# Performance work log

Hardware: AMD Instinct MI355X
Metric: run time of the kernel (lower is better)

The kernel has to match this reference:

```python
import jax, jax.numpy as jnp
import numpy as np

N, C, F, T = 8, 4, 257, 2000
B = 8            # spatial_filters (beams)
M = 80           # spectra_filters
EPS = 1e-5


def setup_inputs() -> dict:
    key = jax.random.key(0)
    ks = jax.random.split(key, 10)
    scale = 0.1
    return {
        "x_real": jax.random.normal(ks[0], (N, C, F, T), jnp.float32),
        "x_imag": jax.random.normal(ks[1], (N, C, F, T), jnp.float32),
        # query beamformer (1 beam): conv weights per bin, shape (F, 1, C)
        "wq_r": jax.random.normal(ks[2], (F, 1, C), jnp.float32) * scale,
        "wq_i": jax.random.normal(ks[3], (F, 1, C), jnp.float32) * scale,
        # key/value beamformers: (F, B, C)
        "wk_r": jax.random.normal(ks[4], (F, B, C), jnp.float32) * scale,
        "wk_i": jax.random.normal(ks[5], (F, B, C), jnp.float32) * scale,
        "wv_r": jax.random.normal(ks[6], (F, B, C), jnp.float32) * scale,
        "wv_i": jax.random.normal(ks[7], (F, B, C), jnp.float32) * scale,
        # spectra projection Linear(F -> M, bias=False): torch weight (M, F)
        "proj_w": jax.random.normal(ks[8], (M, F), jnp.float32) * (1.0 / np.sqrt(F)),
        # BatchNorm1d(M) affine params
        "bn_gamma": jnp.ones((M,), jnp.float32),
        "bn_beta": jnp.zeros((M,), jnp.float32),
    }


def _complex_beam_abs(xr, xi, wr, wi):
    # xr/xi: (N,T,F,C); wr/wi: (F,Beams,C)
    # grouped per-bin conv with kernel==length reduces to contraction over C
    rr = jnp.einsum("ntfc,fbc->ntfb", xr, wr)
    ii = jnp.einsum("ntfc,fbc->ntfb", xi, wi)
    ri = jnp.einsum("ntfc,fbc->ntfb", xi, wr)
    ir = jnp.einsum("ntfc,fbc->ntfb", xr, wi)
    br = rr - ii
    bi = ri + ir
    return jnp.sqrt(br * br + bi * bi + EPS)


def reference(x_real, x_imag, wq_r, wq_i, wk_r, wk_i, wv_r, wv_i, proj_w, bn_gamma, bn_beta):
    # N,C,F,T -> N,T,F,C
    xr = jnp.transpose(x_real, (0, 3, 2, 1))
    xi = jnp.transpose(x_imag, (0, 3, 2, 1))
    bq = _complex_beam_abs(xr, xi, wq_r, wq_i)[..., 0]   # (N,T,F)
    bk = _complex_beam_abs(xr, xi, wk_r, wk_i)           # (N,T,F,B)
    bv = _complex_beam_abs(xr, xi, wv_r, wv_i)           # (N,T,F,B)
    s = jnp.sum(bq[..., None] * bk, axis=-2)             # (N,T,B)
    s = jnp.mean(s, axis=-2, keepdims=True)              # (N,1,B) time-invariant
    w = jax.nn.softmax(s, axis=-1)                       # (N,1,B)
    v = jnp.sum(w[:, None] * bv, axis=-1)                # (N,T,F)
    f = jax.nn.relu(jnp.einsum("ntf,mf->ntm", v, proj_w))
    f = jnp.log(f + EPS)                                 # (N,T,M)
    # BatchNorm1d over channel dim M, training-mode batch stats (biased var)
    mu = jnp.mean(f, axis=(0, 1))
    var = jnp.var(f, axis=(0, 1))
    f = (f - mu) * jax.lax.rsqrt(var + EPS) * bn_gamma + bn_beta
    return f
```

## Files before the change

### kernel.cpp

```cpp
#include <hip/hip_runtime.h>
#include <math.h>

#define NN 8
#define CC 4
#define FF 257
#define TT 2000
#define BB 8
#define MM 80
#define EPSF 1e-5f
#define T4N 500
#define PTILE 32
#define PSTR 260
#define PCHUNK 63

typedef float v2f __attribute__((ext_vector_type(2)));

__device__ __forceinline__ float fsqrt_fast(float x) { return __builtin_amdgcn_sqrtf(x); }
__device__ __forceinline__ float flog_fast(float x)  { return __builtin_amdgcn_logf(x) * 0.69314718055994531f; }
__device__ __forceinline__ v2f sqrt2(v2f m) {
    v2f r; r.x = __builtin_amdgcn_sqrtf(m.x); r.y = __builtin_amdgcn_sqrtf(m.y); return r;
}

__global__ __launch_bounds__(256) void k_beam_s(
    const float* __restrict__ xr_g, const float* __restrict__ xi_g,
    const float* __restrict__ wq_r, const float* __restrict__ wq_i,
    const float* __restrict__ wk_r, const float* __restrict__ wk_i,
    float* __restrict__ s_buf)
{
    int nf = blockIdx.x;
    int n = nf / FF, f = nf % FF;
    int t4 = blockIdx.y * 256 + threadIdx.x;

    float part[BB];
#pragma unroll
    for (int b = 0; b < BB; ++b) part[b] = 0.f;

    if (t4 < T4N) {
        const float* xr_base = xr_g + ((size_t)(n*CC)*FF + f) * TT + t4*4;
        const float* xi_base = xi_g + ((size_t)(n*CC)*FF + f) * TT + t4*4;
        v2f xr2[CC][2], xi2[CC][2];
#pragma unroll
        for (int c = 0; c < CC; ++c) {
            float4 r4 = *reinterpret_cast<const float4*>(xr_base + (size_t)c*FF*TT);
            float4 i4 = *reinterpret_cast<const float4*>(xi_base + (size_t)c*FF*TT);
            xr2[c][0].x = r4.x; xr2[c][0].y = r4.y; xr2[c][1].x = r4.z; xr2[c][1].y = r4.w;
            xi2[c][0].x = i4.x; xi2[c][0].y = i4.y; xi2[c][1].x = i4.z; xi2[c][1].y = i4.w;
        }

        const float4 qr4 = *reinterpret_cast<const float4*>(&wq_r[f*CC]);
        const float4 qi4 = *reinterpret_cast<const float4*>(&wq_i[f*CC]);

        v2f qq[2];
#pragma unroll
        for (int p = 0; p < 2; ++p) {
            v2f qr = xr2[0][p]*qr4.x + xr2[1][p]*qr4.y + xr2[2][p]*qr4.z + xr2[3][p]*qr4.w
                   - xi2[0][p]*qi4.x - xi2[1][p]*qi4.y - xi2[2][p]*qi4.z - xi2[3][p]*qi4.w;
            v2f qi = xi2[0][p]*qr4.x + xi2[1][p]*qr4.y + xi2[2][p]*qr4.z + xi2[3][p]*qr4.w
                   + xr2[0][p]*qi4.x + xr2[1][p]*qi4.y + xr2[2][p]*qi4.z + xr2[3][p]*qi4.w;
            qq[p] = qr*qr + qi*qi + EPSF;
        }

#pragma unroll
        for (int b = 0; b < BB; ++b) {
            const float4 wr4 = *reinterpret_cast<const float4*>(&wk_r[(f*BB + b)*CC]);
            const float4 wi4 = *reinterpret_cast<const float4*>(&wk_i[(f*BB + b)*CC]);
            v2f acc; acc.x = 0.f; acc.y = 0.f;
#pragma unroll
            for (int p = 0; p < 2; ++p) {
                v2f kr = xr2[0][p]*wr4.x + xr2[1][p]*wr4.y + xr2[2][p]*wr4.z + xr2[3][p]*wr4.w
                       - xi2[0][p]*wi4.x - xi2[1][p]*wi4.y - xi2[2][p]*wi4.z - xi2[3][p]*wi4.w;
                v2f ki = xi2[0][p]*wr4.x + xi2[1][p]*wr4.y + xi2[2][p]*wr4.z + xi2[3][p]*wr4.w
                       + xr2[0][p]*wi4.x + xr2[1][p]*wi4.y + xr2[2][p]*wi4.z + xr2[3][p]*wi4.w;
                v2f kk = kr*kr + ki*ki + EPSF;
                acc += sqrt2(qq[p] * kk);
            }
            part[b] = acc.x + acc.y;
        }
    }

    __shared__ float red[4][BB];
    int lane = threadIdx.x & 63, wv = threadIdx.x >> 6;
#pragma unroll
    for (int b = 0; b < BB; ++b) {
        float v = part[b];
#pragma unroll
        for (int m = 32; m >= 1; m >>= 1) v += __shfl_xor(v, m);
        if (lane == 0) red[wv][b] = v;
    }
    __syncthreads();
    if (threadIdx.x < BB) {
        float v = red[0][threadIdx.x] + red[1][threadIdx.x]
                + red[2][threadIdx.x] + red[3][threadIdx.x];
        int bin = (blockIdx.x * 2 + blockIdx.y) & 15;
        atomicAdd(&s_buf[bin*64 + n*BB + threadIdx.x], v);
    }
}

__global__ void k_softmax(const float* __restrict__ s_buf, float* __restrict__ w_buf)
{
    int tid = threadIdx.x;
    if (tid < NN*BB) {
        float v = 0.f;
#pragma unroll
        for (int j = 0; j < 16; ++j) v += s_buf[j*64 + tid];
        v *= (1.0f / TT);
        float mx = v;
#pragma unroll
        for (int m = 4; m >= 1; m >>= 1) mx = fmaxf(mx, __shfl_xor(mx, m));
        float e = expf(v - mx);
        float sm = e;
#pragma unroll
        for (int m = 4; m >= 1; m >>= 1) sm += __shfl_xor(sm, m);
        w_buf[tid] = e / sm;
    }
}

__global__ void k_prep(const float* __restrict__ proj_w, float* __restrict__ proj_pad)
{
    int i = blockIdx.x * 256 + threadIdx.x;
    if (i < MM * 260) {
        int m = i / 260, f = i % 260;
        proj_pad[i] = (f < FF) ? proj_w[m*FF + f] : 0.f;
    }
}

__global__ __launch_bounds__(256) void k_vcompute(
    const float* __restrict__ xr_g, const float* __restrict__ xi_g,
    const float* __restrict__ wv_r, const float* __restrict__ wv_i,
    const float* __restrict__ w_buf, float* __restrict__ vbuf)
{
    int nf = blockIdx.x;
    int n = nf / FF, f = nf % FF;
    int t4 = blockIdx.y * 256 + threadIdx.x;
    if (t4 >= T4N) return;

    const float* xr_base = xr_g + ((size_t)(n*CC)*FF + f) * TT + t4*4;
    const float* xi_base = xi_g + ((size_t)(n*CC)*FF + f) * TT + t4*4;
    v2f xr2[CC][2], xi2[CC][2];
#pragma unroll
    for (int c = 0; c < CC; ++c) {
        float4 r4 = *reinterpret_cast<const float4*>(xr_base + (size_t)c*FF*TT);
        float4 i4 = *reinterpret_cast<const float4*>(xi_base + (size_t)c*FF*TT);
        xr2[c][0].x = r4.x; xr2[c][0].y = r4.y; xr2[c][1].x = r4.z; xr2[c][1].y = r4.w;
        xi2[c][0].x = i4.x; xi2[c][0].y = i4.y; xi2[c][1].x = i4.z; xi2[c][1].y = i4.w;
    }

    v2f vo[2];
    vo[0].x = 0.f; vo[0].y = 0.f; vo[1].x = 0.f; vo[1].y = 0.f;
#pragma unroll
    for (int b = 0; b < BB; ++b) {
        float wn = w_buf[n*BB + b];
        const float4 wr4 = *reinterpret_cast<const float4*>(&wv_r[(f*BB + b)*CC]);
        const float4 wi4 = *reinterpret_cast<const float4*>(&wv_i[(f*BB + b)*CC]);
#pragma unroll
        for (int p = 0; p < 2; ++p) {
            v2f vr = xr2[0][p]*wr4.x + xr2[1][p]*wr4.y + xr2[2][p]*wr4.z + xr2[3][p]*wr4.w
                   - xi2[0][p]*wi4.x - xi2[1][p]*wi4.y - xi2[2][p]*wi4.z - xi2[3][p]*wi4.w;
            v2f vi = xi2[0][p]*wr4.x + xi2[1][p]*wr4.y + xi2[2][p]*wr4.z + xi2[3][p]*wr4.w
                   + xr2[0][p]*wi4.x + xr2[1][p]*wi4.y + xr2[2][p]*wi4.z + xr2[3][p]*wi4.w;
            vo[p] += wn * sqrt2(vr*vr + vi*vi + EPSF);
        }
    }
    float4 o; o.x = vo[0].x; o.y = vo[0].y; o.z = vo[1].x; o.w = vo[1].y;
    *reinterpret_cast<float4*>(&vbuf[((size_t)(n*FF + f))*TT + t4*4]) = o;
}

__global__ __launch_bounds__(256) void k_proj(
    const float* __restrict__ vbuf, const float* __restrict__ proj_pad,
    float* __restrict__ out, double* __restrict__ bn_sum, double* __restrict__ bn_sumsq)
{
    __shared__ float v_lds[PTILE * PSTR];
    int n = blockIdx.x, chunk = blockIdx.y;
    int t0 = chunk * PTILE;
    int tid = threadIdx.x;
    bool full = (t0 + PTILE <= TT);

    if (tid < PTILE*3) {
        int t = tid / 3, fp = FF + tid % 3;
        v_lds[t*PSTR + fp] = 0.f;
    }

    int tq = tid & 7, fi = tid >> 3;
    bool tqv = full || (tq < 4);
#pragma unroll
    for (int k = 0; k < 8; ++k) {
        int f = fi + 32*k;
        float4 vv;
        if (tqv) vv = *reinterpret_cast<const float4*>(&vbuf[((size_t)(n*FF + f))*TT + t0 + tq*4]);
        else { vv.x = 0.f; vv.y = 0.f; vv.z = 0.f; vv.w = 0.f; }
        v_lds[(tq*4 + 0)*PSTR + f] = vv.x;
        v_lds[(tq*4 + 1)*PSTR + f] = vv.y;
        v_lds[(tq*4 + 2)*PSTR + f] = vv.z;
        v_lds[(tq*4 + 3)*PSTR + f] = vv.w;
    }
    if (tid < 8) {
        float4 vv;
        if (full || tid < 4) vv = *reinterpret_cast<const float4*>(&vbuf[((size_t)(n*FF + 256))*TT + t0 + tid*4]);
        else { vv.x = 0.f; vv.y = 0.f; vv.z = 0.f; vv.w = 0.f; }
        v_lds[(tid*4 + 0)*PSTR + 256] = vv.x;
        v_lds[(tid*4 + 1)*PSTR + 256] = vv.y;
        v_lds[(tid*4 + 2)*PSTR + 256] = vv.z;
        v_lds[(tid*4 + 3)*PSTR + 256] = vv.w;
    }
    __syncthreads();

    int tl = tid & 7, fg = tid >> 3;
    int mstart = (fg >> 1)*5 + ((fg & 1) ? 3 : 0);
    bool three = !(fg & 1);

    v2f acc[3][4];
#pragma unroll
    for (int mi = 0; mi < 3; ++mi)
#pragma unroll
        for (int j = 0; j < 4; ++j) { acc[mi][j].x = 0.f; acc[mi][j].y = 0.f; }

    const float* pp = proj_pad + mstart*260;
#pragma unroll 2
    for (int f4 = 0; f4 < 260; f4 += 4) {
        float4 p0 = *reinterpret_cast<const float4*>(&pp[f4]);
        float4 p1 = *reinterpret_cast<const float4*>(&pp[260 + f4]);
        v2f q00, q01, q10, q11, q20, q21;
        q00.x = p0.x; q00.y = p0.y; q01.x = p0.z; q01.y = p0.w;
        q10.x = p1.x; q10.y = p1.y; q11.x = p1.z; q11.y = p1.w;
        if (three) {
            float4 p2 = *reinterpret_cast<const float4*>(&pp[520 + f4]);
            q20.x = p2.x; q20.y = p2.y; q21.x = p2.z; q21.y = p2.w;
        }
#pragma unroll
        for (int j = 0; j < 4; ++j) {
            float4 vv = *reinterpret_cast<const float4*>(&v_lds[(tl + 8*j)*PSTR + f4]);
            v2f v0, v1;
            v0.x = vv.x; v0.y = vv.y; v1.x = vv.z; v1.y = vv.w;
            acc[0][j] += v0*q00 + v1*q01;
            acc[1][j] += v0*q10 + v1*q11;
            if (three) acc[2][j] += v0*q20 + v1*q21;
        }
    }

    int bin = chunk & 15;
#pragma unroll
    for (int mi = 0; mi < 3; ++mi) {
        if (mi == 2 && !three) break;
        int m = mstart + mi;
        float s1 = 0.f, s2 = 0.f;
#pragma unroll
        for (int j = 0; j < 4; ++j) {
            int t = t0 + tl + 8*j;
            if (t < TT) {
                float r = flog_fast(fmaxf(acc[mi][j].x + acc[mi][j].y, 0.f) + EPSF);
                s1 += r; s2 += r*r;
                out[((size_t)n*TT + t)*MM + m] = r;
            }
        }
#pragma unroll
        for (int msk = 4; msk >= 1; msk >>= 1) {
            s1 += __shfl_xor(s1, msk);
            s2 += __shfl_xor(s2, msk);
        }
        if (tl == 0) {
            atomicAdd(&bn_sum[bin*MM + m], (double)s1);
            atomicAdd(&bn_sumsq[bin*MM + m], (double)s2);
        }
    }
}

__global__ void k_bnprep(const double* __restrict__ bn_sum, const double* __restrict__ bn_sumsq,
                         const float* __restrict__ gamma, const float* __restrict__ beta,
                         float* __restrict__ scale, float* __restrict__ shift)
{
    int m = threadIdx.x;
    if (m < MM) {
        double s = 0.0, q = 0.0;
#pragma unroll
        for (int j = 0; j < 16; ++j) { s += bn_sum[j*MM + m]; q += bn_sumsq[j*MM + m]; }
        double inv = 1.0 / (double)(NN * TT);
        double mu = s * inv;
        double var = q * inv - mu * mu;
        float sc = gamma[m] * rsqrtf((float)var + EPSF);
        scale[m] = sc;
        shift[m] = beta[m] - (float)mu * sc;
    }
}

__global__ __launch_bounds__(256) void k_bnapply(float* __restrict__ out,
                                                 const float* __restrict__ scale,
                                                 const float* __restrict__ shift)
{
    int i4 = blockIdx.x * 256 + threadIdx.x;
    if (i4 < NN*TT*MM/4) {
        float4 v = *reinterpret_cast<const float4*>(&out[i4*4]);
        int m = (i4*4) % MM;
        v.x = v.x*scale[m+0] + shift[m+0];
        v.y = v.y*scale[m+1] + shift[m+1];
        v.z = v.z*scale[m+2] + shift[m+2];
        v.w = v.w*scale[m+3] + shift[m+3];
        *reinterpret_cast<float4*>(&out[i4*4]) = v;
    }
}

extern "C" void kernel_launch(void* const* d_in, const int* in_sizes, int n_in,
                              void* d_out, int out_size, void* d_ws, size_t ws_size,
                              hipStream_t stream)
{
    const float* x_real   = (const float*)d_in[0];
    const float* x_imag   = (const float*)d_in[1];
    const float* wq_r     = (const float*)d_in[2];
    const float* wq_i     = (const float*)d_in[3];
    const float* wk_r     = (const float*)d_in[4];
    const float* wk_i     = (const float*)d_in[5];
    const float* wv_r     = (const float*)d_in[6];
    const float* wv_i     = (const float*)d_in[7];
    const float* proj_w   = (const float*)d_in[8];
    const float* bn_gamma = (const float*)d_in[9];
    const float* bn_beta  = (const float*)d_in[10];
    float* out = (float*)d_out;

    char* ws = (char*)d_ws;
    float*  s_buf    = (float*)(ws + 0);
    float*  w_buf    = (float*)(ws + 4096);
    float*  scale    = (float*)(ws + 4352);
    float*  shift    = (float*)(ws + 4672);
    double* bn_sum   = (double*)(ws + 8192);
    double* bn_sumsq = (double*)(ws + 18432);
    float*  proj_pad = (float*)(ws + 28672);
    float*  vbuf     = (float*)(ws + 112640);

    hipMemsetAsync(d_ws, 0, 28672, stream);

    k_prep<<<(MM*260 + 255)/256, 256, 0, stream>>>(proj_w, proj_pad);

    dim3 g1(NN*FF, 2);
    k_beam_s<<<g1, 256, 0, stream>>>(x_real, x_imag, wq_r, wq_i, wk_r, wk_i, s_buf);

    k_softmax<<<1, 64, 0, stream>>>(s_buf, w_buf);

    k_vcompute<<<g1, 256, 0, stream>>>(x_real, x_imag, wv_r, wv_i, w_buf, vbuf);

    dim3 g3(NN, PCHUNK);
    k_proj<<<g3, 256, 0, stream>>>(vbuf, proj_pad, out, bn_sum, bn_sumsq);

    k_bnprep<<<1, 128, 0, stream>>>(bn_sum, bn_sumsq, bn_gamma, bn_beta, scale, shift);

    k_bnapply<<<(NN*TT*MM/4 + 255)/256, 256, 0, stream>>>(out, scale, shift);
}
```

Measured before the change: 101.2 us.

## Fuse small kernels and apply batch-norm via cooperative grid sync

Cuts seven launches down to three. The proj_w padding moves into the beam-score kernel, and each vcompute block computes the softmax itself. The projection kernel becomes a cooperative launch that syncs the whole grid and then applies the batch-norm scale and shift to its own tile while it is likely still in cache. The beam kernels now process both time halves per thread with a 1D grid, which doubles the work per thread and leaves 6 of 256 threads idle. The goal is to remove launch gaps and one full pass over the output, at the cost of grid-sync overhead, per-block recomputation of the softmax, and fewer blocks in flight for the beam kernels.

```diff
diff --git a/kernel.cpp b/kernel.cpp
--- a/kernel.cpp
+++ b/kernel.cpp
@@ -1,5 +1,8 @@
 #include <hip/hip_runtime.h>
+#include <hip/hip_cooperative_groups.h>
 #include <math.h>
+
+namespace cg = cooperative_groups;
 
 #define NN 8
 #define CC 4
@@ -8,10 +11,10 @@
 #define BB 8
 #define MM 80
 #define EPSF 1e-5f
-#define T4N 500
 #define PTILE 32
 #define PSTR 260
 #define PCHUNK 63
+#define HALF1 1000
 
 typedef float v2f __attribute__((ext_vector_type(2)));
 
@@ -25,39 +28,53 @@
     const float* __restrict__ xr_g, const float* __restrict__ xi_g,
     const float* __restrict__ wq_r, const float* __restrict__ wq_i,
     const float* __restrict__ wk_r, const float* __restrict__ wk_i,
-    float* __restrict__ s_buf)
+    float* __restrict__ s_buf,
+    const float* __restrict__ proj_w, float* __restrict__ proj_pad)
 {
     int nf = blockIdx.x;
+    int tid = threadIdx.x;
+
+    {
+        int i = nf*256 + tid;
+        if (i < MM*260) {
+            int m = i/260, fp = i%260;
+            proj_pad[i] = (fp < FF) ? proj_w[m*FF + fp] : 0.f;
+        }
+    }
+
     int n = nf / FF, f = nf % FF;
-    int t4 = blockIdx.y * 256 + threadIdx.x;
 
     float part[BB];
 #pragma unroll
     for (int b = 0; b < BB; ++b) part[b] = 0.f;
 
-    if (t4 < T4N) {
-        const float* xr_base = xr_g + ((size_t)(n*CC)*FF + f) * TT + t4*4;
-        const float* xi_base = xi_g + ((size_t)(n*CC)*FF + f) * TT + t4*4;
-        v2f xr2[CC][2], xi2[CC][2];
+    if (tid < 250) {
+        size_t base0 = ((size_t)(n*CC)*FF + f)*TT + tid*4;
+        v2f xr2[CC][2][2], xi2[CC][2][2];
 #pragma unroll
         for (int c = 0; c < CC; ++c) {
-            float4 r4 = *reinterpret_cast<const float4*>(xr_base + (size_t)c*FF*TT);
-            float4 i4 = *reinterpret_cast<const float4*>(xi_base + (size_t)c*FF*TT);
-            xr2[c][0].x = r4.x; xr2[c][0].y = r4.y; xr2[c][1].x = r4.z; xr2[c][1].y = r4.w;
-            xi2[c][0].x = i4.x; xi2[c][0].y = i4.y; xi2[c][1].x = i4.z; xi2[c][1].y = i4.w;
+#pragma unroll
+            for (int h = 0; h < 2; ++h) {
+                float4 r4 = *reinterpret_cast<const float4*>(xr_g + base0 + (size_t)c*FF*TT + h*HALF1);
+                float4 i4 = *reinterpret_cast<const float4*>(xi_g + base0 + (size_t)c*FF*TT + h*HALF1);
+                xr2[c][h][0].x = r4.x; xr2[c][h][0].y = r4.y; xr2[c][h][1].x = r4.z; xr2[c][h][1].y = r4.w;
+                xi2[c][h][0].x = i4.x; xi2[c][h][0].y = i4.y; xi2[c][h][1].x = i4.z; xi2[c][h][1].y = i4.w;
+            }
         }
 
         const float4 qr4 = *reinterpret_cast<const float4*>(&wq_r[f*CC]);
         const float4 qi4 = *reinterpret_cast<const float4*>(&wq_i[f*CC]);
 
-        v2f qq[2];
+        v2f qq[2][2];
+#pragma unroll
+        for (int h = 0; h < 2; ++h)
 #pragma unroll
         for (int p = 0; p < 2; ++p) {
-            v2f qr = xr2[0][p]*qr4.x + xr2[1][p]*qr4.y + xr2[2][p]*qr4.z + xr2[3][p]*qr4.w
-                   - xi2[0][p]*qi4.x - xi2[1][p]*qi4.y - xi2[2][p]*qi4.z - xi2[3][p]*qi4.w;
-            v2f qi = xi2[0][p]*qr4.x + xi2[1][p]*qr4.y + xi2[2][p]*qr4.z + xi2[3][p]*qr4.w
-                   + xr2[0][p]*qi4.x + xr2[1][p]*qi4.y + xr2[2][p]*qi4.z + xr2[3][p]*qi4.w;
-            qq[p] = qr*qr + qi*qi + EPSF;
+            v2f qr = xr2[0][h][p]*qr4.x + xr2[1][h][p]*qr4.y + xr2[2][h][p]*qr4.z + xr2[3][h][p]*qr4.w
+                   - xi2[0][h][p]*qi4.x - xi2[1][h][p]*qi4.y - xi2[2][h][p]*qi4.z - xi2[3][h][p]*qi4.w;
+            v2f qi = xi2[0][h][p]*qr4.x + xi2[1][h][p]*qr4.y + xi2[2][h][p]*qr4.z + xi2[3][h][p]*qr4.w
+                   + xr2[0][h][p]*qi4.x + xr2[1][h][p]*qi4.y + xr2[2][h][p]*qi4.z + xr2[3][h][p]*qi4.w;
+            qq[h][p] = qr*qr + qi*qi + EPSF;
         }
 
 #pragma unroll
@@ -66,13 +83,15 @@
             const float4 wi4 = *reinterpret_cast<const float4*>(&wk_i[(f*BB + b)*CC]);
             v2f acc; acc.x = 0.f; acc.y = 0.f;
 #pragma unroll
+            for (int h = 0; h < 2; ++h)
+#pragma unroll
             for (int p = 0; p < 2; ++p) {
-                v2f kr = xr2[0][p]*wr4.x + xr2[1][p]*wr4.y + xr2[2][p]*wr4.z + xr2[3][p]*wr4.w
-                       - xi2[0][p]*wi4.x - xi2[1][p]*wi4.y - xi2[2][p]*wi4.z - xi2[3][p]*wi4.w;
-                v2f ki = xi2[0][p]*wr4.x + xi2[1][p]*wr4.y + xi2[2][p]*wr4.z + xi2[3][p]*wr4.w
-                       + xr2[0][p]*wi4.x + xr2[1][p]*wi4.y + xr2[2][p]*wi4.z + xr2[3][p]*wi4.w;
+                v2f kr = xr2[0][h][p]*wr4.x + xr2[1][h][p]*wr4.y + xr2[2][h][p]*wr4.z + xr2[3][h][p]*wr4.w
+                       - xi2[0][h][p]*wi4.x - xi2[1][h][p]*wi4.y - xi2[2][h][p]*wi4.z - xi2[3][h][p]*wi4.w;
+                v2f ki = xi2[0][h][p]*wr4.x + xi2[1][h][p]*wr4.y + xi2[2][h][p]*wr4.z + xi2[3][h][p]*wr4.w
+                       + xr2[0][h][p]*wi4.x + xr2[1][h][p]*wi4.y + xr2[2][h][p]*wi4.z + xr2[3][h][p]*wi4.w;
                 v2f kk = kr*kr + ki*ki + EPSF;
-                acc += sqrt2(qq[p] * kk);
+                acc += sqrt2(qq[h][p] * kk);
             }
             part[b] = acc.x + acc.y;
         }
@@ -91,85 +110,89 @@
     if (threadIdx.x < BB) {
         float v = red[0][threadIdx.x] + red[1][threadIdx.x]
                 + red[2][threadIdx.x] + red[3][threadIdx.x];
-        int bin = (blockIdx.x * 2 + blockIdx.y) & 15;
+        int bin = nf & 15;
         atomicAdd(&s_buf[bin*64 + n*BB + threadIdx.x], v);
-    }
-}
-
-__global__ void k_softmax(const float* __restrict__ s_buf, float* __restrict__ w_buf)
-{
-    int tid = threadIdx.x;
-    if (tid < NN*BB) {
-        float v = 0.f;
-#pragma unroll
-        for (int j = 0; j < 16; ++j) v += s_buf[j*64 + tid];
-        v *= (1.0f / TT);
-        float mx = v;
-#pragma unroll
-        for (int m = 4; m >= 1; m >>= 1) mx = fmaxf(mx, __shfl_xor(mx, m));
-        float e = expf(v - mx);
-        float sm = e;
-#pragma unroll
-        for (int m = 4; m >= 1; m >>= 1) sm += __shfl_xor(sm, m);
-        w_buf[tid] = e / sm;
-    }
-}
-
-__global__ void k_prep(const float* __restrict__ proj_w, float* __restrict__ proj_pad)
-{
-    int i = blockIdx.x * 256 + threadIdx.x;
-    if (i < MM * 260) {
-        int m = i / 260, f = i % 260;
-        proj_pad[i] = (f < FF) ? proj_w[m*FF + f] : 0.f;
     }
 }
 
 __global__ __launch_bounds__(256) void k_vcompute(
     const float* __restrict__ xr_g, const float* __restrict__ xi_g,
     const float* __restrict__ wv_r, const float* __restrict__ wv_i,
-    const float* __restrict__ w_buf, float* __restrict__ vbuf)
+    const float* __restrict__ s_buf, float* __restrict__ vbuf)
 {
     int nf = blockIdx.x;
     int n = nf / FF, f = nf % FF;
-    int t4 = blockIdx.y * 256 + threadIdx.x;
-    if (t4 >= T4N) return;
-
-    const float* xr_base = xr_g + ((size_t)(n*CC)*FF + f) * TT + t4*4;
-    const float* xi_base = xi_g + ((size_t)(n*CC)*FF + f) * TT + t4*4;
-    v2f xr2[CC][2], xi2[CC][2];
+    int tid = threadIdx.x;
+
+    float wn[BB];
+    {
+        float sv[BB]; float mx = -1e30f;
+#pragma unroll
+        for (int b = 0; b < BB; ++b) {
+            float v = 0.f;
+#pragma unroll
+            for (int j = 0; j < 16; ++j) v += s_buf[j*64 + n*BB + b];
+            sv[b] = v * (1.0f / TT);
+            mx = fmaxf(mx, sv[b]);
+        }
+        float sm = 0.f;
+#pragma unroll
+        for (int b = 0; b < BB; ++b) { sv[b] = expf(sv[b] - mx); sm += sv[b]; }
+        float inv = 1.0f / sm;
+#pragma unroll
+        for (int b = 0; b < BB; ++b) wn[b] = sv[b] * inv;
+    }
+
+    if (tid >= 250) return;
+    size_t base0 = ((size_t)(n*CC)*FF + f)*TT + tid*4;
+    v2f xr2[CC][2][2], xi2[CC][2][2];
 #pragma unroll
     for (int c = 0; c < CC; ++c) {
-        float4 r4 = *reinterpret_cast<const float4*>(xr_base + (size_t)c*FF*TT);
-        float4 i4 = *reinterpret_cast<const float4*>(xi_base + (size_t)c*FF*TT);
-        xr2[c][0].x = r4.x; xr2[c][0].y = r4.y; xr2[c][1].x = r4.z; xr2[c][1].y = r4.w;
-        xi2[c][0].x = i4.x; xi2[c][0].y = i4.y; xi2[c][1].x = i4.z; xi2[c][1].y = i4.w;
-    }
-
-    v2f vo[2];
-    vo[0].x = 0.f; vo[0].y = 0.f; vo[1].x = 0.f; vo[1].y = 0.f;
+#pragma unroll
+        for (int h = 0; h < 2; ++h) {
+            float4 r4 = *reinterpret_cast<const float4*>(xr_g + base0 + (size_t)c*FF*TT + h*HALF1);
+            float4 i4 = *reinterpret_cast<const float4*>(xi_g + base0 + (size_t)c*FF*TT + h*HALF1);
+            xr2[c][h][0].x = r4.x; xr2[c][h][0].y = r4.y; xr2[c][h][1].x = r4.z; xr2[c][h][1].y = r4.w;
+            xi2[c][h][0].x = i4.x; xi2[c][h][0].y = i4.y; xi2[c][h][1].x = i4.z; xi2[c][h][1].y = i4.w;
+        }
+    }
+
+    v2f vo[2][2];
+#pragma unroll
+    for (int h = 0; h < 2; ++h)
+#pragma unroll
+    for (int p = 0; p < 2; ++p) { vo[h][p].x = 0.f; vo[h][p].y = 0.f; }
+
 #pragma unroll
     for (int b = 0; b < BB; ++b) {
-        float wn = w_buf[n*BB + b];
         const float4 wr4 = *reinterpret_cast<const float4*>(&wv_r[(f*BB + b)*CC]);
         const float4 wi4 = *reinterpret_cast<const float4*>(&wv_i[(f*BB + b)*CC]);
+        float wnb = wn[b];
+#pragma unroll
+        for (int h = 0; h < 2; ++h)
 #pragma unroll
         for (int p = 0; p < 2; ++p) {
-            v2f vr = xr2[0][p]*wr4.x + xr2[1][p]*wr4.y + xr2[2][p]*wr4.z + xr2[3][p]*wr4.w
-                   - xi2[0][p]*wi4.x - xi2[1][p]*wi4.y - xi2[2][p]*wi4.z - xi2[3][p]*wi4.w;
-            v2f vi = xi2[0][p]*wr4.x + xi2[1][p]*wr4.y + xi2[2][p]*wr4.z + xi2[3][p]*wr4.w
-                   + xr2[0][p]*wi4.x + xr2[1][p]*wi4.y + xr2[2][p]*wi4.z + xr2[3][p]*wi4.w;
-            vo[p] += wn * sqrt2(vr*vr + vi*vi + EPSF);
-        }
-    }
-    float4 o; o.x = vo[0].x; o.y = vo[0].y; o.z = vo[1].x; o.w = vo[1].y;
-    *reinterpret_cast<float4*>(&vbuf[((size_t)(n*FF + f))*TT + t4*4]) = o;
+            v2f vr = xr2[0][h][p]*wr4.x + xr2[1][h][p]*wr4.y + xr2[2][h][p]*wr4.z + xr2[3][h][p]*wr4.w
+                   - xi2[0][h][p]*wi4.x - xi2[1][h][p]*wi4.y - xi2[2][h][p]*wi4.z - xi2[3][h][p]*wi4.w;
+            v2f vi = xi2[0][h][p]*wr4.x + xi2[1][h][p]*wr4.y + xi2[2][h][p]*wr4.z + xi2[3][h][p]*wr4.w
+                   + xr2[0][h][p]*wi4.x + xr2[1][h][p]*wi4.y + xr2[2][h][p]*wi4.z + xr2[3][h][p]*wi4.w;
+            vo[h][p] += wnb * sqrt2(vr*vr + vi*vi + EPSF);
+        }
+    }
+#pragma unroll
+    for (int h = 0; h < 2; ++h) {
+        float4 o; o.x = vo[h][0].x; o.y = vo[h][0].y; o.z = vo[h][1].x; o.w = vo[h][1].y;
+        *reinterpret_cast<float4*>(&vbuf[((size_t)(n*FF + f))*TT + tid*4 + h*HALF1]) = o;
+    }
 }
 
 __global__ __launch_bounds__(256) void k_proj(
     const float* __restrict__ vbuf, const float* __restrict__ proj_pad,
-    float* __restrict__ out, double* __restrict__ bn_sum, double* __restrict__ bn_sumsq)
+    float* __restrict__ out, double* __restrict__ bn_sum, double* __restrict__ bn_sumsq,
+    const float* __restrict__ gamma, const float* __restrict__ beta)
 {
     __shared__ float v_lds[PTILE * PSTR];
+    __shared__ float sc_l[MM], sh_l[MM];
     int n = blockIdx.x, chunk = blockIdx.y;
     int t0 = chunk * PTILE;
     int tid = threadIdx.x;
@@ -262,39 +285,36 @@
             atomicAdd(&bn_sumsq[bin*MM + m], (double)s2);
         }
     }
-}
-
-__global__ void k_bnprep(const double* __restrict__ bn_sum, const double* __restrict__ bn_sumsq,
-                         const float* __restrict__ gamma, const float* __restrict__ beta,
-                         float* __restrict__ scale, float* __restrict__ shift)
-{
-    int m = threadIdx.x;
-    if (m < MM) {
+
+    cg::this_grid().sync();
+
+    if (tid < MM) {
         double s = 0.0, q = 0.0;
 #pragma unroll
-        for (int j = 0; j < 16; ++j) { s += bn_sum[j*MM + m]; q += bn_sumsq[j*MM + m]; }
+        for (int j = 0; j < 16; ++j) {
+            s += __hip_atomic_load(&bn_sum[j*MM + tid], __ATOMIC_RELAXED, __HIP_MEMORY_SCOPE_AGENT);
+            q += __hip_atomic_load(&bn_sumsq[j*MM + tid], __ATOMIC_RELAXED, __HIP_MEMORY_SCOPE_AGENT);
+        }
         double inv = 1.0 / (double)(NN * TT);
         double mu = s * inv;
         double var = q * inv - mu * mu;
-        float sc = gamma[m] * rsqrtf((float)var + EPSF);
-        scale[m] = sc;
-        shift[m] = beta[m] - (float)mu * sc;
-    }
-}
-
-__global__ __launch_bounds__(256) void k_bnapply(float* __restrict__ out,
-                                                 const float* __restrict__ scale,
-                                                 const float* __restrict__ shift)
-{
-    int i4 = blockIdx.x * 256 + threadIdx.x;
-    if (i4 < NN*TT*MM/4) {
-        float4 v = *reinterpret_cast<const float4*>(&out[i4*4]);
-        int m = (i4*4) % MM;
-        v.x = v.x*scale[m+0] + shift[m+0];
-        v.y = v.y*scale[m+1] + shift[m+1];
-        v.z = v.z*scale[m+2] + shift[m+2];
-        v.w = v.w*scale[m+3] + shift[m+3];
-        *reinterpret_cast<float4*>(&out[i4*4]) = v;
+        float sc = gamma[tid] * rsqrtf((float)var + EPSF);
+        sc_l[tid] = sc;
+        sh_l[tid] = beta[tid] - (float)mu * sc;
+    }
+    __syncthreads();
+
+    int tn = full ? PTILE : (TT - t0);
+    float* tile = out + ((size_t)n*TT + t0)*MM;
+    int len4 = tn*MM/4;
+    for (int k = tid; k < len4; k += 256) {
+        float4 v = *reinterpret_cast<const float4*>(tile + k*4);
+        int m = (k*4) % MM;
+        v.x = v.x*sc_l[m+0] + sh_l[m+0];
+        v.y = v.y*sc_l[m+1] + sh_l[m+1];
+        v.z = v.z*sc_l[m+2] + sh_l[m+2];
+        v.w = v.w*sc_l[m+3] + sh_l[m+3];
+        *reinterpret_cast<float4*>(tile + k*4) = v;
     }
 }
 
@@ -317,9 +337,6 @@
 
     char* ws = (char*)d_ws;
     float*  s_buf    = (float*)(ws + 0);
-    float*  w_buf    = (float*)(ws + 4096);
-    float*  scale    = (float*)(ws + 4352);
-    float*  shift    = (float*)(ws + 4672);
     double* bn_sum   = (double*)(ws + 8192);
     double* bn_sumsq = (double*)(ws + 18432);
     float*  proj_pad = (float*)(ws + 28672);
@@ -327,19 +344,15 @@
 
     hipMemsetAsync(d_ws, 0, 28672, stream);
 
-    k_prep<<<(MM*260 + 255)/256, 256, 0, stream>>>(proj_w, proj_pad);
-
-    dim3 g1(NN*FF, 2);
-    k_beam_s<<<g1, 256, 0, stream>>>(x_real, x_imag, wq_r, wq_i, wk_r, wk_i, s_buf);
-
-    k_softmax<<<1, 64, 0, stream>>>(s_buf, w_buf);
-
-    k_vcompute<<<g1, 256, 0, stream>>>(x_real, x_imag, wv_r, wv_i, w_buf, vbuf);
-
-    dim3 g3(NN, PCHUNK);
-    k_proj<<<g3, 256, 0, stream>>>(vbuf, proj_pad, out, bn_sum, bn_sumsq);
-
-    k_bnprep<<<1, 128, 0, stream>>>(bn_sum, bn_sumsq, bn_gamma, bn_beta, scale, shift);
-
-    k_bnapply<<<(NN*TT*MM/4 + 255)/256, 256, 0, stream>>>(out, scale, shift);
-}
+    dim3 g1(NN*FF, 1);
+    k_beam_s<<<g1, 256, 0, stream>>>(x_real, x_imag, wq_r, wq_i, wk_r, wk_i, s_buf,
+                                     proj_w, proj_pad);
+
+    k_vcompute<<<g1, 256, 0, stream>>>(x_real, x_imag, wv_r, wv_i, s_buf, vbuf);
+
+    void* args[] = { (void*)&vbuf, (void*)&proj_pad, (void*)&out,
+                     (void*)&bn_sum, (void*)&bn_sumsq,
+                     (void*)&bn_gamma, (void*)&bn_beta };
+    hipLaunchCooperativeKernel((const void*)k_proj, dim3(NN, PCHUNK), dim3(256),
+                               args, 0, stream);
+}
```

After: 162.1 us. 1.6x slower.

## Fold tiny prep, softmax and BN-stat kernels into neighbouring kernels

Applied to the files above, without the earlier changes.

Removes three small launches: proj_w padding moves into k_beam_s (blockIdx.y==0 blocks), the softmax is recomputed redundantly per thread inside k_vcompute from s_buf, and BN stat finalization is done per block in shared memory inside the apply kernel. This cuts launch overhead and serialization gaps between dependent tiny kernels. In exchange every vcompute thread reads 128 s_buf values and computes 8 exps, and every bnapply block re-reduces 16x80 doubles.

```diff
diff --git a/kernel.cpp b/kernel.cpp
--- a/kernel.cpp
+++ b/kernel.cpp
@@ -25,9 +25,18 @@
     const float* __restrict__ xr_g, const float* __restrict__ xi_g,
     const float* __restrict__ wq_r, const float* __restrict__ wq_i,
     const float* __restrict__ wk_r, const float* __restrict__ wk_i,
-    float* __restrict__ s_buf)
+    float* __restrict__ s_buf,
+    const float* __restrict__ proj_w, float* __restrict__ proj_pad)
 {
     int nf = blockIdx.x;
+    if (blockIdx.y == 0) {
+        int i = nf*256 + threadIdx.x;
+        if (i < MM*260) {
+            int m = i/260, fp = i%260;
+            proj_pad[i] = (fp < FF) ? proj_w[m*FF + fp] : 0.f;
+        }
+    }
+
     int n = nf / FF, f = nf % FF;
     int t4 = blockIdx.y * 256 + threadIdx.x;
 
@@ -96,43 +105,34 @@
     }
 }
 
-__global__ void k_softmax(const float* __restrict__ s_buf, float* __restrict__ w_buf)
-{
-    int tid = threadIdx.x;
-    if (tid < NN*BB) {
-        float v = 0.f;
-#pragma unroll
-        for (int j = 0; j < 16; ++j) v += s_buf[j*64 + tid];
-        v *= (1.0f / TT);
-        float mx = v;
-#pragma unroll
-        for (int m = 4; m >= 1; m >>= 1) mx = fmaxf(mx, __shfl_xor(mx, m));
-        float e = expf(v - mx);
-        float sm = e;
-#pragma unroll
-        for (int m = 4; m >= 1; m >>= 1) sm += __shfl_xor(sm, m);
-        w_buf[tid] = e / sm;
-    }
-}
-
-__global__ void k_prep(const float* __restrict__ proj_w, float* __restrict__ proj_pad)
-{
-    int i = blockIdx.x * 256 + threadIdx.x;
-    if (i < MM * 260) {
-        int m = i / 260, f = i % 260;
-        proj_pad[i] = (f < FF) ? proj_w[m*FF + f] : 0.f;
-    }
-}
-
 __global__ __launch_bounds__(256) void k_vcompute(
     const float* __restrict__ xr_g, const float* __restrict__ xi_g,
     const float* __restrict__ wv_r, const float* __restrict__ wv_i,
-    const float* __restrict__ w_buf, float* __restrict__ vbuf)
+    const float* __restrict__ s_buf, float* __restrict__ vbuf)
 {
     int nf = blockIdx.x;
     int n = nf / FF, f = nf % FF;
     int t4 = blockIdx.y * 256 + threadIdx.x;
     if (t4 >= T4N) return;
+
+    float wn[BB];
+    {
+        float sv[BB]; float mx = -1e30f;
+#pragma unroll
+        for (int b = 0; b < BB; ++b) {
+            float v = 0.f;
+#pragma unroll
+            for (int j = 0; j < 16; ++j) v += s_buf[j*64 + n*BB + b];
+            sv[b] = v * (1.0f / TT);
+            mx = fmaxf(mx, sv[b]);
+        }
+        float sm = 0.f;
+#pragma unroll
+        for (int b = 0; b < BB; ++b) { sv[b] = expf(sv[b] - mx); sm += sv[b]; }
+        float inv = 1.0f / sm;
+#pragma unroll
+        for (int b = 0; b < BB; ++b) wn[b] = sv[b] * inv;
+    }
 
     const float* xr_base = xr_g + ((size_t)(n*CC)*FF + f) * TT + t4*4;
     const float* xi_base = xi_g + ((size_t)(n*CC)*FF + f) * TT + t4*4;
@@ -149,16 +149,16 @@
     vo[0].x = 0.f; vo[0].y = 0.f; vo[1].x = 0.f; vo[1].y = 0.f;
 #pragma unroll
     for (int b = 0; b < BB; ++b) {
-        float wn = w_buf[n*BB + b];
         const float4 wr4 = *reinterpret_cast<const float4*>(&wv_r[(f*BB + b)*CC]);
         const float4 wi4 = *reinterpret_cast<const float4*>(&wv_i[(f*BB + b)*CC]);
+        float wnb = wn[b];
 #pragma unroll
         for (int p = 0; p < 2; ++p) {
             v2f vr = xr2[0][p]*wr4.x + xr2[1][p]*wr4.y + xr2[2][p]*wr4.z + xr2[3][p]*wr4.w
                    - xi2[0][p]*wi4.x - xi2[1][p]*wi4.y - xi2[2][p]*wi4.z - xi2[3][p]*wi4.w;
             v2f vi = xi2[0][p]*wr4.x + xi2[1][p]*wr4.y + xi2[2][p]*wr4.z + xi2[3][p]*wr4.w
                    + xr2[0][p]*wi4.x + xr2[1][p]*wi4.y + xr2[2][p]*wi4.z + xr2[3][p]*wi4.w;
-            vo[p] += wn * sqrt2(vr*vr + vi*vi + EPSF);
+            vo[p] += wnb * sqrt2(vr*vr + vi*vi + EPSF);
         }
     }
     float4 o; o.x = vo[0].x; o.y = vo[0].y; o.z = vo[1].x; o.w = vo[1].y;
@@ -264,36 +264,35 @@
     }
 }
 
-__global__ void k_bnprep(const double* __restrict__ bn_sum, const double* __restrict__ bn_sumsq,
-                         const float* __restrict__ gamma, const float* __restrict__ beta,
-                         float* __restrict__ scale, float* __restrict__ shift)
-{
-    int m = threadIdx.x;
-    if (m < MM) {
+__global__ __launch_bounds__(256) void k_bnfuse(float* __restrict__ out,
+                                                const double* __restrict__ bn_sum,
+                                                const double* __restrict__ bn_sumsq,
+                                                const float* __restrict__ gamma,
+                                                const float* __restrict__ beta)
+{
+    __shared__ float sc_l[MM], sh_l[MM];
+    int tid = threadIdx.x;
+    if (tid < MM) {
         double s = 0.0, q = 0.0;
 #pragma unroll
-        for (int j = 0; j < 16; ++j) { s += bn_sum[j*MM + m]; q += bn_sumsq[j*MM + m]; }
+        for (int j = 0; j < 16; ++j) { s += bn_sum[j*MM + tid]; q += bn_sumsq[j*MM + tid]; }
         double inv = 1.0 / (double)(NN * TT);
         double mu = s * inv;
         double var = q * inv - mu * mu;
-        float sc = gamma[m] * rsqrtf((float)var + EPSF);
-        scale[m] = sc;
-        shift[m] = beta[m] - (float)mu * sc;
-    }
-}
-
-__global__ __launch_bounds__(256) void k_bnapply(float* __restrict__ out,
-                                                 const float* __restrict__ scale,
-                                                 const float* __restrict__ shift)
-{
-    int i4 = blockIdx.x * 256 + threadIdx.x;
+        float sc = gamma[tid] * rsqrtf((float)var + EPSF);
+        sc_l[tid] = sc;
+        sh_l[tid] = beta[tid] - (float)mu * sc;
+    }
+    __syncthreads();
+
+    int i4 = blockIdx.x * 256 + tid;
     if (i4 < NN*TT*MM/4) {
         float4 v = *reinterpret_cast<const float4*>(&out[i4*4]);
         int m = (i4*4) % MM;
-        v.x = v.x*scale[m+0] + shift[m+0];
-        v.y = v.y*scale[m+1] + shift[m+1];
-        v.z = v.z*scale[m+2] + shift[m+2];
-        v.w = v.w*scale[m+3] + shift[m+3];
+        v.x = v.x*sc_l[m+0] + sh_l[m+0];
+        v.y = v.y*sc_l[m+1] + sh_l[m+1];
+        v.z = v.z*sc_l[m+2] + sh_l[m+2];
+        v.w = v.w*sc_l[m+3] + sh_l[m+3];
         *reinterpret_cast<float4*>(&out[i4*4]) = v;
     }
 }
@@ -317,9 +316,6 @@
 
     char* ws = (char*)d_ws;
     float*  s_buf    = (float*)(ws + 0);
-    float*  w_buf    = (float*)(ws + 4096);
-    float*  scale    = (float*)(ws + 4352);
-    float*  shift    = (float*)(ws + 4672);
     double* bn_sum   = (double*)(ws + 8192);
     double* bn_sumsq = (double*)(ws + 18432);
     float*  proj_pad = (float*)(ws + 28672);
@@ -327,19 +323,15 @@
 
     hipMemsetAsync(d_ws, 0, 28672, stream);
 
-    k_prep<<<(MM*260 + 255)/256, 256, 0, stream>>>(proj_w, proj_pad);
-
     dim3 g1(NN*FF, 2);
-    k_beam_s<<<g1, 256, 0, stream>>>(x_real, x_imag, wq_r, wq_i, wk_r, wk_i, s_buf);
-
-    k_softmax<<<1, 64, 0, stream>>>(s_buf, w_buf);
-
-    k_vcompute<<<g1, 256, 0, stream>>>(x_real, x_imag, wv_r, wv_i, w_buf, vbuf);
+    k_beam_s<<<g1, 256, 0, stream>>>(x_real, x_imag, wq_r, wq_i, wk_r, wk_i, s_buf,
+                                     proj_w, proj_pad);
+
+    k_vcompute<<<g1, 256, 0, stream>>>(x_real, x_imag, wv_r, wv_i, s_buf, vbuf);
 
     dim3 g3(NN, PCHUNK);
     k_proj<<<g3, 256, 0, stream>>>(vbuf, proj_pad, out, bn_sum, bn_sumsq);
 
-    k_bnprep<<<1, 128, 0, stream>>>(bn_sum, bn_sumsq, bn_gamma, bn_beta, scale, shift);
-
-    k_bnapply<<<(NN*TT*MM/4 + 255)/256, 256, 0, stream>>>(out, scale, shift);
-}
+    k_bnfuse<<<(NN*TT*MM/4 + 255)/256, 256, 0, stream>>>(out, bn_sum, bn_sumsq,
+                                                          bn_gamma, bn_beta);
+}
```

After: 98.20 us. 1.03x faster.
